# Kernel optimization log

Hardware: AMD Instinct MI355X
Metric: run time of the kernel (lower is better)

## Reference

```python
import jax, jax.numpy as jnp
import numpy as np

# Gemma3-style config (matches init_kwargs)
NUM_HEADS = 8
NUM_KV_GROUPS = 4
HEAD_DIM = 256
GROUP_SIZE = NUM_HEADS // NUM_KV_GROUPS
SLIDING_WINDOW = 1024
QUERY_PRE_ATTN_SCALAR = 256.0
SCALE = QUERY_PRE_ATTN_SCALAR ** (-0.5)
EPS = 1e-6


def rmsnorm(x, scale):
    # Gemma-style RMSNorm: fp32 variance, zero-centered weight with (1 + scale)
    xf = x.astype(jnp.float32)
    var = jnp.mean(xf * xf, axis=-1, keepdims=True)
    out = xf * jax.lax.rsqrt(var + EPS) * (1.0 + scale.astype(jnp.float32))
    return out.astype(x.dtype)


def sliding_causal_mask(q_len, kv_len, dtype):
    # additive mask [q_len, kv_len]: 0 allowed, -inf blocked
    q_pos = jnp.arange(kv_len - q_len, kv_len)[:, None]
    k_pos = jnp.arange(kv_len)[None, :]
    allowed = (k_pos <= q_pos) & (k_pos >= q_pos - SLIDING_WINDOW + 1)
    return jnp.where(allowed, jnp.zeros((), dtype), jnp.array(-jnp.inf, dtype))


def setup_inputs() -> dict:
    key = jax.random.key(0)
    ks = jax.random.split(key, 5)
    B, T, D = 2, 2048, 2560
    H, G, Hd = NUM_HEADS, NUM_KV_GROUPS, HEAD_DIM
    x = jax.random.normal(ks[0], (B, T, D), dtype=jnp.float32)
    Wq = jax.random.normal(ks[1], (D, H * Hd), dtype=jnp.float32) * 0.02
    Wk = jax.random.normal(ks[2], (D, G * Hd), dtype=jnp.float32) * 0.02
    Wv = jax.random.normal(ks[3], (D, G * Hd), dtype=jnp.float32) * 0.02
    Wo = jax.random.normal(ks[4], (H * Hd, D), dtype=jnp.float32) * 0.02
    q_scale = jnp.zeros((Hd,), dtype=jnp.float32)
    k_scale = jnp.zeros((Hd,), dtype=jnp.float32)
    return {"x": x, "Wq": Wq, "Wk": Wk, "Wv": Wv, "Wo": Wo,
            "q_scale": q_scale, "k_scale": k_scale}


def reference(x, Wq, Wk, Wv, Wo, q_scale, k_scale):
    B, T, D = x.shape
    H, G, g, Hd = NUM_HEADS, NUM_KV_GROUPS, GROUP_SIZE, HEAD_DIM
    # projections
    q = (x @ Wq).reshape(B, T, H, Hd).transpose(0, 2, 1, 3)   # [B,H,T,Hd]
    k = (x @ Wk).reshape(B, T, G, Hd).transpose(0, 2, 1, 3)   # [B,G,T,Hd]
    v = (x @ Wv).reshape(B, T, G, Hd).transpose(0, 2, 1, 3)   # [B,G,T,Hd]
    # qk-norm
    q = rmsnorm(q, q_scale)
    k = rmsnorm(k, k_scale)
    S = T  # no past_kv (prefill)
    # faithful reproduction of the module's head-group reshapes
    q = q.reshape(B, G, g, T, Hd).reshape(B * g, G, T, Hd)
    k = jnp.broadcast_to(k[:, None], (B, g, G, S, Hd)).reshape(B * g, G, S, Hd)
    v = jnp.broadcast_to(v[:, None], (B, g, G, S, Hd)).reshape(B * g, G, S, Hd)
    mask = sliding_causal_mask(T, S, q.dtype)  # [T,S]
    scores = jnp.einsum('bgtd,bgsd->bgts', q, k) * SCALE + mask
    attn = jax.nn.softmax(scores, axis=-1)
    out = jnp.einsum('bgts,bgsd->bgtd', attn, v)
    # faithful inverse reshapes (note g/G order swap vs input, as in source)
    out = out.reshape(B, g, G, T, Hd).reshape(B, H, T, Hd)
    out = out.transpose(0, 2, 1, 3).reshape(B, T, H * Hd)
    return out @ Wo
```

## Files before the change

### kernel.cpp

```cpp
#include <hip/hip_runtime.h>
#include <hip/hip_bf16.h>

typedef unsigned short u16;

#define T_SEQ 2048
#define NTOK 4096
#define D_MODEL 2560
#define NQKV 4096
#define WIN 1024
#define ATTN_SCALE 0.0625f
#define SMAX 17.0f
#define KROW 264
#define VROW 40

typedef __attribute__((ext_vector_type(8))) short bf16x8;
typedef __attribute__((ext_vector_type(8))) unsigned short u16x8;
typedef __attribute__((ext_vector_type(4))) float f32x4;

__device__ __forceinline__ float bf2f(u16 u) {
  union { unsigned int i; float f; } c; c.i = ((unsigned int)u) << 16; return c.f;
}
__device__ __forceinline__ u16 f2bf(float f) {
  __hip_bfloat16 h = __float2bfloat16(f);
  return __builtin_bit_cast(u16, h);
}
__device__ __forceinline__ u16x8 load8f(const float* p) {
  float4 a = *(const float4*)p;
  float4 b = *(const float4*)(p + 4);
  u16x8 r;
  r[0] = f2bf(a.x); r[1] = f2bf(a.y); r[2] = f2bf(a.z); r[3] = f2bf(a.w);
  r[4] = f2bf(b.x); r[5] = f2bf(b.y); r[6] = f2bf(b.z); r[7] = f2bf(b.w);
  return r;
}
__device__ __forceinline__ void gload_lds16(const u16* g, u16* l) {
  __builtin_amdgcn_global_load_lds(
      (const __attribute__((address_space(1))) void*)g,
      (__attribute__((address_space(3))) void*)l, 16, 0, 0);
}

__global__ __launch_bounds__(256) void cvt_f32_bf16(
    const float* __restrict__ in, u16* __restrict__ out) {
  size_t i = ((size_t)blockIdx.x * 256 + threadIdx.x) * 8;
  *(u16x8*)(out + i) = load8f(in + i);
}

__global__ __launch_bounds__(256) void transpose_w(
    const float* __restrict__ in, u16* __restrict__ out, int K, int N) {
  __shared__ u16 tile[64][65];
  int kb = blockIdx.y * 64, nb = blockIdx.x * 64;
  int t = threadIdx.x;
  int c4 = (t & 15) * 4;
  int r0 = t >> 4;
#pragma unroll
  for (int i = 0; i < 4; ++i) {
    int r = r0 + i * 16;
    float4 v = *(const float4*)(in + (size_t)(kb + r) * N + nb + c4);
    tile[r][c4] = f2bf(v.x); tile[r][c4 + 1] = f2bf(v.y);
    tile[r][c4 + 2] = f2bf(v.z); tile[r][c4 + 3] = f2bf(v.w);
  }
  __syncthreads();
#pragma unroll
  for (int i = 0; i < 4; ++i) {
    int n = r0 + i * 16;
    ushort4 v;
    v.x = tile[c4 + 0][n];
    v.y = tile[c4 + 1][n];
    v.z = tile[c4 + 2][n];
    v.w = tile[c4 + 3][n];
    *(ushort4*)(out + (size_t)(nb + n) * K + kb + c4) = v;
  }
}

__global__ __launch_bounds__(256) void v_transpose(
    const u16* __restrict__ qkv, u16* __restrict__ Vt) {
  int bg = blockIdx.z; int b = bg >> 2, g = bg & 3;
  __shared__ u16 tile[64][65];
  int tb = blockIdx.y * 64, db = blockIdx.x * 64;
  const u16* in = qkv + (size_t)(b * T_SEQ) * NQKV + 3072 + g * 256;
  u16* out = Vt + (size_t)bg * 256 * T_SEQ;
  int t = threadIdx.x;
  int c4 = (t & 15) * 4;
  int r0 = t >> 4;
#pragma unroll
  for (int i = 0; i < 4; ++i) {
    int r = r0 + i * 16;
    ushort4 v = *(const ushort4*)(in + (size_t)(tb + r) * NQKV + db + c4);
    tile[r][c4] = v.x; tile[r][c4 + 1] = v.y; tile[r][c4 + 2] = v.z; tile[r][c4 + 3] = v.w;
  }
  __syncthreads();
#pragma unroll
  for (int i = 0; i < 4; ++i) {
    int n = r0 + i * 16;
    ushort4 v;
    v.x = tile[c4 + 0][n];
    v.y = tile[c4 + 1][n];
    v.z = tile[c4 + 2][n];
    v.w = tile[c4 + 3][n];
    *(ushort4*)(out + (size_t)(db + n) * T_SEQ + tb + c4) = v;
  }
}

template <int WC>
__global__ __launch_bounds__(512, 2) void gemm_256(
    const u16* __restrict__ A, int lda, const u16* __restrict__ Bt, int ldb,
    void* __restrict__ C, int ldc, int K) {
  extern __shared__ ulong2 LDSraw[];
  u16* SA = (u16*)LDSraw;
  u16* SB = SA + 32768;
  const int tid = threadIdx.x;
  const int wave = tid >> 6, lane = tid & 63;
  const int quad = lane >> 4, l16 = lane & 15;
  const int gx = gridDim.x;
  const int orig = blockIdx.y * gx + blockIdx.x;
  const int cpx = (gx * gridDim.y) >> 3;
  const int swz = (orig & 7) * cpx + (orig >> 3);
  const int mblk = (swz / gx) * 256, nblk = (swz % gx) * 256;
  const int wm = (wave >> 2) * 128, wn = (wave & 3) * 64;

  const u16* srcA[2]; const u16* srcB[2];
  int ldsOff[2];
#pragma unroll
  for (int i = 0; i < 2; ++i) {
    int u = i * 512 + tid;
    int hi3 = (u & 7) ^ ((u >> 3) & 7);
    int r = ((u >> 3) << 1) | (hi3 >> 2);
    int cbe = (hi3 & 3) << 3;
    srcA[i] = A + (size_t)(mblk + r) * lda + cbe;
    srcB[i] = Bt + (size_t)(nblk + r) * ldb + cbe;
    ldsOff[i] = (u >> 6) << 9;
  }
  const int unit = ((((l16 & 1) << 2) | quad) ^ ((l16 >> 1) & 7)) << 3;
  const int base_a = ((wm >> 1) + (l16 >> 1)) * 64 + unit;
  const int base_b = ((wn >> 1) + (l16 >> 1)) * 64 + unit;
  const int NK = K >> 5;
  f32x4 acc[8][4] = {};

  auto stage = [&](int s, int i) {
    int slot = s & 3;
    gload_lds16(srcA[i] + s * 32, SA + slot * 8192 + ldsOff[i]);
    gload_lds16(srcB[i] + s * 32, SB + slot * 8192 + ldsOff[i]);
  };

  stage(0, 0); stage(0, 1); stage(1, 0); stage(1, 1); stage(2, 0); stage(2, 1);
  asm volatile("s_waitcnt vmcnt(8)" ::: "memory");
  __builtin_amdgcn_s_barrier();
  asm volatile("" ::: "memory");

  for (int s = 0; s < NK; ++s) {
    const u16* sa = SA + (s & 3) * 8192;
    const u16* sb = SB + (s & 3) * 8192;
    bf16x8 aF[4], bF[4];
#pragma unroll
    for (int t = 0; t < 4; ++t) aF[t] = *(const bf16x8*)(sa + base_a + t * 512);
#pragma unroll
    for (int t = 0; t < 4; ++t) bF[t] = *(const bf16x8*)(sb + base_b + t * 512);
    if (s + 3 < NK) stage(s + 3, 0);
    asm volatile("" ::: "memory");
    __builtin_amdgcn_s_barrier();
    asm volatile("s_waitcnt lgkmcnt(0)" ::: "memory");
    __builtin_amdgcn_sched_barrier(0);
    __builtin_amdgcn_s_setprio(1);
#pragma unroll
    for (int n = 0; n < 4; ++n)
#pragma unroll
      for (int m = 0; m < 4; ++m)
        acc[m][n] = __builtin_amdgcn_mfma_f32_16x16x32_bf16(aF[m], bF[n], acc[m][n], 0, 0, 0);
    __builtin_amdgcn_s_setprio(0);
    asm volatile("" ::: "memory");
    __builtin_amdgcn_s_barrier();
    asm volatile("" ::: "memory");
#pragma unroll
    for (int t = 0; t < 4; ++t) aF[t] = *(const bf16x8*)(sa + base_a + (t + 4) * 512);
    if (s + 3 < NK) stage(s + 3, 1);
    asm volatile("" ::: "memory");
    __builtin_amdgcn_s_barrier();
    asm volatile("s_waitcnt lgkmcnt(0)" ::: "memory");
    __builtin_amdgcn_sched_barrier(0);
    __builtin_amdgcn_s_setprio(1);
#pragma unroll
    for (int n = 0; n < 4; ++n)
#pragma unroll
      for (int m = 0; m < 4; ++m)
        acc[m + 4][n] = __builtin_amdgcn_mfma_f32_16x16x32_bf16(aF[m], bF[n], acc[m + 4][n], 0, 0, 0);
    __builtin_amdgcn_s_setprio(0);
    if (s < NK - 3)       asm volatile("s_waitcnt vmcnt(6)" ::: "memory");
    else if (s == NK - 3) asm volatile("s_waitcnt vmcnt(4)" ::: "memory");
    else if (s == NK - 2) asm volatile("s_waitcnt vmcnt(0)" ::: "memory");
    if (s + 1 < NK) {
      asm volatile("" ::: "memory");
      __builtin_amdgcn_s_barrier();
      asm volatile("" ::: "memory");
    }
  }
#pragma unroll
  for (int m = 0; m < 8; ++m)
#pragma unroll
    for (int n = 0; n < 4; ++n)
#pragma unroll
      for (int r = 0; r < 4; ++r) {
        int row = mblk + wm + m * 16 + quad * 4 + r;
        int col = nblk + wn + n * 16 + l16;
        if constexpr (WC)
          ((float*)C)[(size_t)row * ldc + col] = acc[m][n][r];
        else
          ((u16*)C)[(size_t)row * ldc + col] = f2bf(acc[m][n][r]);
      }
}

template <int WC>
__global__ __launch_bounds__(256, 2) void gemm_fast(
    const u16* __restrict__ A, int lda, const u16* __restrict__ Bt, int ldb,
    void* __restrict__ C, int ldc, int K) {
  __shared__ __align__(16) u16 As[128 * 32];
  __shared__ __align__(16) u16 Bs[128 * 32];
  const int tid = threadIdx.x;
  const int wave = tid >> 6, lane = tid & 63;
  const int quad = lane >> 4, l16 = lane & 15;
  const int mblk = blockIdx.y * 128, nblk = blockIdx.x * 128;
  const int wm = (wave >> 1) * 64, wn = (wave & 1) * 64;
  f32x4 acc[4][4] = {};
  const int c0 = wave * 2;
  for (int k0 = 0; k0 < K; k0 += 32) {
#pragma unroll
    for (int i = 0; i < 2; ++i) {
      int c = c0 + i;
      int flat = c * 64 + lane;
      int row = flat >> 2;
      int kb = (flat & 3) * 8;
      gload_lds16(A + (size_t)(mblk + row) * lda + k0 + kb, As + c * 512);
      gload_lds16(Bt + (size_t)(nblk + row) * ldb + k0 + kb, Bs + c * 512);
    }
    __syncthreads();
    bf16x8 aF[4], bF[4];
#pragma unroll
    for (int t = 0; t < 4; ++t) {
      aF[t] = *(const bf16x8*)(As + (wm + t * 16 + l16) * 32 + quad * 8);
      bF[t] = *(const bf16x8*)(Bs + (wn + t * 16 + l16) * 32 + quad * 8);
    }
#pragma unroll
    for (int tm = 0; tm < 4; ++tm)
#pragma unroll
      for (int tn = 0; tn < 4; ++tn)
        acc[tm][tn] = __builtin_amdgcn_mfma_f32_16x16x32_bf16(aF[tm], bF[tn], acc[tm][tn], 0, 0, 0);
    __syncthreads();
  }
#pragma unroll
  for (int tm = 0; tm < 4; ++tm)
#pragma unroll
    for (int tn = 0; tn < 4; ++tn)
#pragma unroll
      for (int r = 0; r < 4; ++r) {
        int row = mblk + wm + tm * 16 + quad * 4 + r;
        int col = nblk + wn + tn * 16 + l16;
        if constexpr (WC)
          ((float*)C)[(size_t)row * ldc + col] = acc[tm][tn][r];
        else
          ((u16*)C)[(size_t)row * ldc + col] = f2bf(acc[tm][tn][r]);
      }
}

__global__ __launch_bounds__(256, 2) void gemm_f32a(
    const float* __restrict__ A, int lda, const u16* __restrict__ Bt, int ldb,
    u16* __restrict__ C, int ldc, int K) {
  __shared__ __align__(16) u16 As[128 * 32];
  __shared__ __align__(16) u16 Bs[128 * 32];
  const int tid = threadIdx.x;
  const int wave = tid >> 6, lane = tid & 63;
  const int quad = lane >> 4, l16 = lane & 15;
  const int mblk = blockIdx.y * 128, nblk = blockIdx.x * 128;
  const int wm = (wave >> 1) * 64, wn = (wave & 1) * 64;
  f32x4 acc[4][4] = {};
  for (int k0 = 0; k0 < K; k0 += 32) {
#pragma unroll
    for (int i = 0; i < 2; ++i) {
      int u = i * 256 + tid;
      int row = u >> 2;
      int kb = (u & 3) * 8;
      *(u16x8*)(As + row * 32 + kb) = load8f(A + (size_t)(mblk + row) * lda + k0 + kb);
      *(u16x8*)(Bs + row * 32 + kb) = *(const u16x8*)(Bt + (size_t)(nblk + row) * ldb + k0 + kb);
    }
    __syncthreads();
    bf16x8 aF[4], bF[4];
#pragma unroll
    for (int t = 0; t < 4; ++t) {
      aF[t] = *(const bf16x8*)(As + (wm + t * 16 + l16) * 32 + quad * 8);
      bF[t] = *(const bf16x8*)(Bs + (wn + t * 16 + l16) * 32 + quad * 8);
    }
#pragma unroll
    for (int tm = 0; tm < 4; ++tm)
#pragma unroll
      for (int tn = 0; tn < 4; ++tn)
        acc[tm][tn] = __builtin_amdgcn_mfma_f32_16x16x32_bf16(aF[tm], bF[tn], acc[tm][tn], 0, 0, 0);
    __syncthreads();
  }
#pragma unroll
  for (int tm = 0; tm < 4; ++tm)
#pragma unroll
    for (int tn = 0; tn < 4; ++tn)
#pragma unroll
      for (int r = 0; r < 4; ++r) {
        int row = mblk + wm + tm * 16 + quad * 4 + r;
        int col = nblk + wn + tn * 16 + l16;
        C[(size_t)row * ldc + col] = f2bf(acc[tm][tn][r]);
      }
}

__global__ __launch_bounds__(256) void rmsnorm_qk(
    u16* __restrict__ qkv, const float* __restrict__ q_scale,
    const float* __restrict__ k_scale) {
  int wv = blockIdx.x * 4 + (threadIdx.x >> 6);
  int lane = threadIdx.x & 63;
  int token = wv / 12, j = wv - token * 12;
  const float* sc = (j < 8) ? q_scale : k_scale;
  int col = (j < 8) ? j * 256 : 2048 + (j - 8) * 256;
  u16* p = qkv + (size_t)token * NQKV + col;
  int d = lane * 4;
  ushort4 raw = *(const ushort4*)(p + d);
  float x0 = bf2f(raw.x), x1 = bf2f(raw.y), x2 = bf2f(raw.z), x3 = bf2f(raw.w);
  float sum = x0 * x0 + x1 * x1 + x2 * x2 + x3 * x3;
#pragma unroll
  for (int m = 1; m < 64; m <<= 1) sum += __shfl_xor(sum, m, 64);
  float r = rsqrtf(sum * (1.0f / 256.0f) + 1e-6f);
  float4 sv = *(const float4*)(sc + d);
  ushort4 o;
  o.x = f2bf(x0 * r * (1.0f + sv.x));
  o.y = f2bf(x1 * r * (1.0f + sv.y));
  o.z = f2bf(x2 * r * (1.0f + sv.z));
  o.w = f2bf(x3 * r * (1.0f + sv.w));
  *(ushort4*)(p + d) = o;
}

__global__ __launch_bounds__(256) void attn_fused(
    u16* __restrict__ qkv, const u16* __restrict__ Vt) {
  const int qt = blockIdx.x, h = blockIdx.y, b = blockIdx.z;
  const int g = h & 3;
  const int tid = threadIdx.x;
  const int wave = tid >> 6, lane = tid & 63;
  const int quad = lane >> 4, l16 = lane & 15;
  const int t0 = qt * 64;
  const int tw = t0 + wave * 16;
  __shared__ __align__(16) u16 Ks[2][32 * KROW];
  __shared__ __align__(16) u16 Vs[2][256 * VROW];
  __shared__ __align__(16) u16 Ps[4][16 * VROW];
  bf16x8 qF[8];
  {
    const u16* qrow = qkv + (size_t)(b * T_SEQ + tw + l16) * NQKV + h * 256;
#pragma unroll
    for (int kc = 0; kc < 8; ++kc)
      qF[kc] = *(const bf16x8*)(qrow + kc * 32 + quad * 8);
  }
  const u16* vt_base = Vt + (size_t)(b * 4 + g) * 256 * T_SEQ;
  const u16* k_base = qkv + (size_t)(b * T_SEQ) * NQKV + 2048 + g * 256;
  f32x4 o[16] = {};
  float lsum[4] = {0.f, 0.f, 0.f, 0.f};
  int s_lo = t0 - (WIN - 1); if (s_lo < 0) s_lo = 0; s_lo &= ~31;
  const int s_hi = t0 + 63;
  const int n_tiles = (s_hi - s_lo + 32) >> 5;

  u16x8 rK[4], rV[4];
#define ISSUE_LOADS(sb)                                                       \
  {                                                                           \
    _Pragma("unroll")                                                         \
    for (int i = 0; i < 4; ++i) {                                             \
      int u = i * 256 + tid;                                                  \
      int krow = u >> 5, kcb = u & 31;                                        \
      rK[i] = *(const u16x8*)(k_base + (size_t)((sb) + krow) * NQKV + kcb * 8);\
      int dim = u >> 2, kvp = (u & 3) * 8;                                    \
      rV[i] = *(const u16x8*)(vt_base + (size_t)dim * T_SEQ + (sb) + kvp);    \
    }                                                                         \
  }
#define WRITE_LDS(buf)                                                        \
  {                                                                           \
    _Pragma("unroll")                                                         \
    for (int i = 0; i < 4; ++i) {                                             \
      int u = i * 256 + tid;                                                  \
      int krow = u >> 5, kcb = u & 31;                                        \
      *(u16x8*)(Ks[buf] + krow * KROW + kcb * 8) = rK[i];                     \
      int dim = u >> 2, kvp = (u & 3) * 8;                                    \
      *(u16x8*)(Vs[buf] + dim * VROW + kvp) = rV[i];                          \
    }                                                                         \
  }

  ISSUE_LOADS(s_lo);
  WRITE_LDS(0);
  __syncthreads();

  for (int ti = 0; ti < n_tiles; ++ti) {
    const int sb = s_lo + ti * 32;
    const int buf = ti & 1;
    if (ti + 1 < n_tiles) ISSUE_LOADS(sb + 32);
    f32x4 st[2] = {};
#pragma unroll
    for (int nt = 0; nt < 2; ++nt)
#pragma unroll
      for (int kc = 0; kc < 8; ++kc) {
        bf16x8 kF = *(const bf16x8*)(Ks[buf] + (nt * 16 + l16) * KROW + kc * 32 + quad * 8);
        st[nt] = __builtin_amdgcn_mfma_f32_16x16x32_bf16(qF[kc], kF, st[nt], 0, 0, 0);
      }
    const bool full = (sb + 31 <= tw) && (sb >= tw + 15 - (WIN - 1));
#pragma unroll
    for (int r = 0; r < 4; ++r) {
      float v0 = st[0][r] * ATTN_SCALE - SMAX;
      float v1 = st[1][r] * ATTN_SCALE - SMAX;
      if (!full) {
        int t = tw + quad * 4 + r;
        int c0s = sb + l16, c1s = c0s + 16;
        v0 = (c0s <= t && c0s > t - WIN) ? v0 : -3.0e38f;
        v1 = (c1s <= t && c1s > t - WIN) ? v1 : -3.0e38f;
      }
      float p0 = __expf(v0);
      float p1 = __expf(v1);
      Ps[wave][(quad * 4 + r) * VROW + l16] = f2bf(p0);
      Ps[wave][(quad * 4 + r) * VROW + 16 + l16] = f2bf(p1);
      lsum[r] += p0 + p1;
    }
    bf16x8 pF = *(const bf16x8*)(&Ps[wave][l16 * VROW + quad * 8]);
#pragma unroll
    for (int nt = 0; nt < 16; ++nt) {
      bf16x8 vF = *(const bf16x8*)(Vs[buf] + (nt * 16 + l16) * VROW + quad * 8);
      o[nt] = __builtin_amdgcn_mfma_f32_16x16x32_bf16(pF, vF, o[nt], 0, 0, 0);
    }
    if (ti + 1 < n_tiles) WRITE_LDS(buf ^ 1);
    __syncthreads();
  }
#undef ISSUE_LOADS
#undef WRITE_LDS
#pragma unroll
  for (int r = 0; r < 4; ++r) {
    float s = lsum[r];
    s += __shfl_xor(s, 1, 64);
    s += __shfl_xor(s, 2, 64);
    s += __shfl_xor(s, 4, 64);
    s += __shfl_xor(s, 8, 64);
    lsum[r] = s;
  }
#pragma unroll
  for (int r = 0; r < 4; ++r) {
    float inv = 1.0f / lsum[r];
    int t = tw + quad * 4 + r;
    u16* orow = qkv + (size_t)(b * T_SEQ + t) * NQKV + h * 256;
#pragma unroll
    for (int nt = 0; nt < 16; ++nt)
      orow[nt * 16 + l16] = f2bf(o[nt][r] * inv);
  }
}

extern "C" void kernel_launch(void* const* d_in, const int* in_sizes, int n_in,
                              void* d_out, int out_size, void* d_ws, size_t ws_size,
                              hipStream_t stream) {
  const float* x       = (const float*)d_in[0];
  const float* Wq      = (const float*)d_in[1];
  const float* Wk      = (const float*)d_in[2];
  const float* Wv      = (const float*)d_in[3];
  const float* Wo      = (const float*)d_in[4];
  const float* q_scale = (const float*)d_in[5];
  const float* k_scale = (const float*)d_in[6];

  u16* qkv = (u16*)d_ws;
  const size_t BIG_WS = (size_t)NTOK * NQKV * 2
                      + (size_t)NTOK * D_MODEL * 2
                      + (size_t)NQKV * D_MODEL * 2;

  if (ws_size >= BIG_WS) {
    (void)hipFuncSetAttribute(reinterpret_cast<const void*>(&gemm_256<0>),
                              hipFuncAttributeMaxDynamicSharedMemorySize, 131072);
    u16* xbf = qkv + (size_t)NTOK * NQKV;
    u16* WT  = xbf + (size_t)NTOK * D_MODEL;
    cvt_f32_bf16<<<dim3(NTOK * D_MODEL / (256 * 8)), 256, 0, stream>>>(x, xbf);
    transpose_w<<<dim3(32, 40), 256, 0, stream>>>(Wq, WT, D_MODEL, 2048);
    transpose_w<<<dim3(16, 40), 256, 0, stream>>>(Wk, WT + (size_t)2048 * D_MODEL, D_MODEL, 1024);
    transpose_w<<<dim3(16, 40), 256, 0, stream>>>(Wv, WT + (size_t)3072 * D_MODEL, D_MODEL, 1024);
    gemm_256<0><<<dim3(16, 16), 512, 131072, stream>>>(xbf, D_MODEL, WT, D_MODEL, qkv, NQKV, D_MODEL);
    rmsnorm_qk<<<dim3(12288), 256, 0, stream>>>(qkv, q_scale, k_scale);
    v_transpose<<<dim3(4, 32, 8), 256, 0, stream>>>(qkv, xbf);
    attn_fused<<<dim3(T_SEQ / 64, 8, 2), 256, 0, stream>>>(qkv, xbf);
    transpose_w<<<dim3(40, 32), 256, 0, stream>>>(Wo, WT, 2048, D_MODEL);
    gemm_fast<1><<<dim3(20, 32), 256, 0, stream>>>(qkv, NQKV, WT, 2048, d_out, D_MODEL, 2048);
  } else {
    u16* WT = qkv + (size_t)NTOK * NQKV;
    transpose_w<<<dim3(32, 40), 256, 0, stream>>>(Wq, WT, D_MODEL, 2048);
    gemm_f32a<<<dim3(16, 32), 256, 0, stream>>>(x, D_MODEL, WT, D_MODEL, qkv, NQKV, D_MODEL);
    transpose_w<<<dim3(16, 40), 256, 0, stream>>>(Wk, WT, D_MODEL, 1024);
    gemm_f32a<<<dim3(8, 32), 256, 0, stream>>>(x, D_MODEL, WT, D_MODEL, qkv + 2048, NQKV, D_MODEL);
    transpose_w<<<dim3(16, 40), 256, 0, stream>>>(Wv, WT, D_MODEL, 1024);
    gemm_f32a<<<dim3(8, 32), 256, 0, stream>>>(x, D_MODEL, WT, D_MODEL, qkv + 3072, NQKV, D_MODEL);
    rmsnorm_qk<<<dim3(12288), 256, 0, stream>>>(qkv, q_scale, k_scale);
    v_transpose<<<dim3(4, 32, 8), 256, 0, stream>>>(qkv, WT);
    attn_fused<<<dim3(T_SEQ / 64, 8, 2), 256, 0, stream>>>(qkv, WT);
    transpose_w<<<dim3(40, 32), 256, 0, stream>>>(Wo, WT, 2048, D_MODEL);
    gemm_fast<1><<<dim3(20, 32), 256, 0, stream>>>(qkv, NQKV, WT, 2048, d_out, D_MODEL, 2048);
  }
}
```

Baseline: 378.6 us.

## Use 4-wave 256x256 GEMM with 128x128 per-wave tiles for QKV and output projections

Reworks the 256x256-tile GEMM from 8 waves with 128x64 per-wave tiles to 4 waves with 128x128 per-wave tiles. Each wave now holds 64 accumulator tiles and loads 8 A and 8 B fragments per k-step, which raises MFMA work per LDS read. The same kernel also replaces the 128-tile gemm_fast for the output projection, now on a 10x16 grid. The cost is much higher register pressure (launch_bounds 256,1) and fewer waves to hide latency, and the output GEMM launches only 160 blocks, which may underfill the device.

```diff
diff --git a/kernel.cpp b/kernel.cpp
--- a/kernel.cpp
+++ b/kernel.cpp
@@ -101,7 +101,7 @@
 }
 
 template <int WC>
-__global__ __launch_bounds__(512, 2) void gemm_256(
+__global__ __launch_bounds__(256, 1) void gemm_fat(
     const u16* __restrict__ A, int lda, const u16* __restrict__ Bt, int ldb,
     void* __restrict__ C, int ldc, int K) {
   extern __shared__ ulong2 LDSraw[];
@@ -115,13 +115,13 @@
   const int cpx = (gx * gridDim.y) >> 3;
   const int swz = (orig & 7) * cpx + (orig >> 3);
   const int mblk = (swz / gx) * 256, nblk = (swz % gx) * 256;
-  const int wm = (wave >> 2) * 128, wn = (wave & 3) * 64;
-
-  const u16* srcA[2]; const u16* srcB[2];
-  int ldsOff[2];
-#pragma unroll
-  for (int i = 0; i < 2; ++i) {
-    int u = i * 512 + tid;
+  const int wm = (wave >> 1) * 128, wn = (wave & 1) * 128;
+
+  const u16* srcA[4]; const u16* srcB[4];
+  int ldsOff[4];
+#pragma unroll
+  for (int i = 0; i < 4; ++i) {
+    int u = i * 256 + tid;
     int hi3 = (u & 7) ^ ((u >> 3) & 7);
     int r = ((u >> 3) << 1) | (hi3 >> 2);
     int cbe = (hi3 & 3) << 3;
@@ -133,28 +133,33 @@
   const int base_a = ((wm >> 1) + (l16 >> 1)) * 64 + unit;
   const int base_b = ((wn >> 1) + (l16 >> 1)) * 64 + unit;
   const int NK = K >> 5;
-  f32x4 acc[8][4] = {};
-
-  auto stage = [&](int s, int i) {
-    int slot = s & 3;
-    gload_lds16(srcA[i] + s * 32, SA + slot * 8192 + ldsOff[i]);
-    gload_lds16(srcB[i] + s * 32, SB + slot * 8192 + ldsOff[i]);
+  f32x4 acc[8][8] = {};
+
+  auto stageA = [&](int s) {
+    u16* d = SA + (s & 3) * 8192;
+#pragma unroll
+    for (int i = 0; i < 4; ++i) gload_lds16(srcA[i] + s * 32, d + ldsOff[i]);
   };
-
-  stage(0, 0); stage(0, 1); stage(1, 0); stage(1, 1); stage(2, 0); stage(2, 1);
-  asm volatile("s_waitcnt vmcnt(8)" ::: "memory");
+  auto stageB = [&](int s) {
+    u16* d = SB + (s & 3) * 8192;
+#pragma unroll
+    for (int i = 0; i < 4; ++i) gload_lds16(srcB[i] + s * 32, d + ldsOff[i]);
+  };
+
+  stageA(0); stageB(0); stageA(1); stageB(1); stageA(2); stageB(2);
+  asm volatile("s_waitcnt vmcnt(16)" ::: "memory");
   __builtin_amdgcn_s_barrier();
   asm volatile("" ::: "memory");
 
   for (int s = 0; s < NK; ++s) {
     const u16* sa = SA + (s & 3) * 8192;
     const u16* sb = SB + (s & 3) * 8192;
-    bf16x8 aF[4], bF[4];
-#pragma unroll
-    for (int t = 0; t < 4; ++t) aF[t] = *(const bf16x8*)(sa + base_a + t * 512);
+    bf16x8 aF[8], bF[8];
+#pragma unroll
+    for (int t = 0; t < 8; ++t) aF[t] = *(const bf16x8*)(sa + base_a + t * 512);
 #pragma unroll
     for (int t = 0; t < 4; ++t) bF[t] = *(const bf16x8*)(sb + base_b + t * 512);
-    if (s + 3 < NK) stage(s + 3, 0);
+    if (s + 3 < NK) stageA(s + 3);
     asm volatile("" ::: "memory");
     __builtin_amdgcn_s_barrier();
     asm volatile("s_waitcnt lgkmcnt(0)" ::: "memory");
@@ -163,28 +168,28 @@
 #pragma unroll
     for (int n = 0; n < 4; ++n)
 #pragma unroll
-      for (int m = 0; m < 4; ++m)
+      for (int m = 0; m < 8; ++m)
         acc[m][n] = __builtin_amdgcn_mfma_f32_16x16x32_bf16(aF[m], bF[n], acc[m][n], 0, 0, 0);
     __builtin_amdgcn_s_setprio(0);
     asm volatile("" ::: "memory");
     __builtin_amdgcn_s_barrier();
     asm volatile("" ::: "memory");
 #pragma unroll
-    for (int t = 0; t < 4; ++t) aF[t] = *(const bf16x8*)(sa + base_a + (t + 4) * 512);
-    if (s + 3 < NK) stage(s + 3, 1);
+    for (int t = 4; t < 8; ++t) bF[t] = *(const bf16x8*)(sb + base_b + t * 512);
+    if (s + 3 < NK) stageB(s + 3);
     asm volatile("" ::: "memory");
     __builtin_amdgcn_s_barrier();
     asm volatile("s_waitcnt lgkmcnt(0)" ::: "memory");
     __builtin_amdgcn_sched_barrier(0);
     __builtin_amdgcn_s_setprio(1);
 #pragma unroll
-    for (int n = 0; n < 4; ++n)
-#pragma unroll
-      for (int m = 0; m < 4; ++m)
-        acc[m + 4][n] = __builtin_amdgcn_mfma_f32_16x16x32_bf16(aF[m], bF[n], acc[m + 4][n], 0, 0, 0);
+    for (int n = 4; n < 8; ++n)
+#pragma unroll
+      for (int m = 0; m < 8; ++m)
+        acc[m][n] = __builtin_amdgcn_mfma_f32_16x16x32_bf16(aF[m], bF[n], acc[m][n], 0, 0, 0);
     __builtin_amdgcn_s_setprio(0);
-    if (s < NK - 3)       asm volatile("s_waitcnt vmcnt(6)" ::: "memory");
-    else if (s == NK - 3) asm volatile("s_waitcnt vmcnt(4)" ::: "memory");
+    if (s < NK - 3)       asm volatile("s_waitcnt vmcnt(16)" ::: "memory");
+    else if (s == NK - 3) asm volatile("s_waitcnt vmcnt(8)" ::: "memory");
     else if (s == NK - 2) asm volatile("s_waitcnt vmcnt(0)" ::: "memory");
     if (s + 1 < NK) {
       asm volatile("" ::: "memory");
@@ -195,7 +200,7 @@
 #pragma unroll
   for (int m = 0; m < 8; ++m)
 #pragma unroll
-    for (int n = 0; n < 4; ++n)
+    for (int n = 0; n < 8; ++n)
 #pragma unroll
       for (int r = 0; r < 4; ++r) {
         int row = mblk + wm + m * 16 + quad * 4 + r;
@@ -462,7 +467,9 @@
                       + (size_t)NQKV * D_MODEL * 2;
 
   if (ws_size >= BIG_WS) {
-    (void)hipFuncSetAttribute(reinterpret_cast<const void*>(&gemm_256<0>),
+    (void)hipFuncSetAttribute(reinterpret_cast<const void*>(&gemm_fat<0>),
+                              hipFuncAttributeMaxDynamicSharedMemorySize, 131072);
+    (void)hipFuncSetAttribute(reinterpret_cast<const void*>(&gemm_fat<1>),
                               hipFuncAttributeMaxDynamicSharedMemorySize, 131072);
     u16* xbf = qkv + (size_t)NTOK * NQKV;
     u16* WT  = xbf + (size_t)NTOK * D_MODEL;
@@ -470,12 +477,12 @@
     transpose_w<<<dim3(32, 40), 256, 0, stream>>>(Wq, WT, D_MODEL, 2048);
     transpose_w<<<dim3(16, 40), 256, 0, stream>>>(Wk, WT + (size_t)2048 * D_MODEL, D_MODEL, 1024);
     transpose_w<<<dim3(16, 40), 256, 0, stream>>>(Wv, WT + (size_t)3072 * D_MODEL, D_MODEL, 1024);
-    gemm_256<0><<<dim3(16, 16), 512, 131072, stream>>>(xbf, D_MODEL, WT, D_MODEL, qkv, NQKV, D_MODEL);
+    gemm_fat<0><<<dim3(16, 16), 256, 131072, stream>>>(xbf, D_MODEL, WT, D_MODEL, qkv, NQKV, D_MODEL);
     rmsnorm_qk<<<dim3(12288), 256, 0, stream>>>(qkv, q_scale, k_scale);
     v_transpose<<<dim3(4, 32, 8), 256, 0, stream>>>(qkv, xbf);
     attn_fused<<<dim3(T_SEQ / 64, 8, 2), 256, 0, stream>>>(qkv, xbf);
     transpose_w<<<dim3(40, 32), 256, 0, stream>>>(Wo, WT, 2048, D_MODEL);
-    gemm_fast<1><<<dim3(20, 32), 256, 0, stream>>>(qkv, NQKV, WT, 2048, d_out, D_MODEL, 2048);
+    gemm_fat<1><<<dim3(10, 16), 256, 131072, stream>>>(qkv, NQKV, WT, 2048, d_out, D_MODEL, 2048);
   } else {
     u16* WT = qkv + (size_t)NTOK * NQKV;
     transpose_w<<<dim3(32, 40), 256, 0, stream>>>(Wq, WT, D_MODEL, 2048);
```

Result: slower. 389.9 us (+3.0%).

## Restructure QKV GEMM main loop and merge small prep/post kernels

Applied to the files above, without the earlier changes.

The QKV GEMM inner loop now preloads the next step's first A fragments and loads the second half of A with B up front. This cuts the barriers and explicit lgkmcnt waits per K step from four to two, so LDS reads overlap with MFMA work. Separately, the input conversion and Wq/Wk/Wv transposes are merged into one `prep` launch. RMSNorm, the V transpose and the Wo transpose are merged into one `post` launch, removing several kernel launches and the gaps between them. The trade-off is more live fragment registers and looser LDS synchronisation in the GEMM, which could cost occupancy or introduce subtle ordering hazards.

```diff
diff --git a/kernel.cpp b/kernel.cpp
--- a/kernel.cpp
+++ b/kernel.cpp
@@ -38,17 +38,16 @@
       (__attribute__((address_space(3))) void*)l, 16, 0, 0);
 }
 
-__global__ __launch_bounds__(256) void cvt_f32_bf16(
-    const float* __restrict__ in, u16* __restrict__ out) {
-  size_t i = ((size_t)blockIdx.x * 256 + threadIdx.x) * 8;
+__device__ __forceinline__ void cvt_body(
+    const float* __restrict__ in, u16* __restrict__ out, int bid, int t) {
+  size_t i = ((size_t)bid * 256 + t) * 8;
   *(u16x8*)(out + i) = load8f(in + i);
 }
 
-__global__ __launch_bounds__(256) void transpose_w(
-    const float* __restrict__ in, u16* __restrict__ out, int K, int N) {
-  __shared__ u16 tile[64][65];
-  int kb = blockIdx.y * 64, nb = blockIdx.x * 64;
-  int t = threadIdx.x;
+__device__ __forceinline__ void tw_body(
+    const float* __restrict__ in, u16* __restrict__ out, int K, int N,
+    int bx, int by, int t, u16 (*tile)[65]) {
+  int kb = by * 64, nb = bx * 64;
   int c4 = (t & 15) * 4;
   int r0 = t >> 4;
 #pragma unroll
@@ -71,14 +70,13 @@
   }
 }
 
-__global__ __launch_bounds__(256) void v_transpose(
-    const u16* __restrict__ qkv, u16* __restrict__ Vt) {
-  int bg = blockIdx.z; int b = bg >> 2, g = bg & 3;
-  __shared__ u16 tile[64][65];
-  int tb = blockIdx.y * 64, db = blockIdx.x * 64;
+__device__ __forceinline__ void vt_body(
+    const u16* __restrict__ qkv, u16* __restrict__ Vt,
+    int bx, int by, int bg, int t, u16 (*tile)[65]) {
+  int b = bg >> 2, g = bg & 3;
+  int tb = by * 64, db = bx * 64;
   const u16* in = qkv + (size_t)(b * T_SEQ) * NQKV + 3072 + g * 256;
   u16* out = Vt + (size_t)bg * 256 * T_SEQ;
-  int t = threadIdx.x;
   int c4 = (t & 15) * 4;
   int r0 = t >> 4;
 #pragma unroll
@@ -98,6 +96,75 @@
     v.w = tile[c4 + 3][n];
     *(ushort4*)(out + (size_t)(db + n) * T_SEQ + tb + c4) = v;
   }
+}
+
+__device__ __forceinline__ void rms_body(
+    u16* __restrict__ qkv, const float* __restrict__ q_scale,
+    const float* __restrict__ k_scale, int bid, int tidx) {
+  int wv = bid * 4 + (tidx >> 6);
+  int lane = tidx & 63;
+  int token = wv / 12, j = wv - token * 12;
+  const float* sc = (j < 8) ? q_scale : k_scale;
+  int col = (j < 8) ? j * 256 : 2048 + (j - 8) * 256;
+  u16* p = qkv + (size_t)token * NQKV + col;
+  int d = lane * 4;
+  ushort4 raw = *(const ushort4*)(p + d);
+  float x0 = bf2f(raw.x), x1 = bf2f(raw.y), x2 = bf2f(raw.z), x3 = bf2f(raw.w);
+  float sum = x0 * x0 + x1 * x1 + x2 * x2 + x3 * x3;
+#pragma unroll
+  for (int m = 1; m < 64; m <<= 1) sum += __shfl_xor(sum, m, 64);
+  float r = rsqrtf(sum * (1.0f / 256.0f) + 1e-6f);
+  float4 sv = *(const float4*)(sc + d);
+  ushort4 o;
+  o.x = f2bf(x0 * r * (1.0f + sv.x));
+  o.y = f2bf(x1 * r * (1.0f + sv.y));
+  o.z = f2bf(x2 * r * (1.0f + sv.z));
+  o.w = f2bf(x3 * r * (1.0f + sv.w));
+  *(ushort4*)(p + d) = o;
+}
+
+__global__ __launch_bounds__(256) void prep(
+    const float* __restrict__ x, u16* __restrict__ xbf,
+    const float* __restrict__ Wq, const float* __restrict__ Wk,
+    const float* __restrict__ Wv, u16* __restrict__ WT) {
+  __shared__ u16 tile[64][65];
+  int id = blockIdx.x, t = threadIdx.x;
+  if (id < 5120) { cvt_body(x, xbf, id, t); return; }
+  id -= 5120;
+  if (id < 1280) { tw_body(Wq, WT, D_MODEL, 2048, id % 32, id / 32, t, tile); return; }
+  id -= 1280;
+  if (id < 640) { tw_body(Wk, WT + (size_t)2048 * D_MODEL, D_MODEL, 1024, id % 16, id / 16, t, tile); return; }
+  id -= 640;
+  tw_body(Wv, WT + (size_t)3072 * D_MODEL, D_MODEL, 1024, id % 16, id / 16, t, tile);
+}
+
+__global__ __launch_bounds__(256) void post(
+    u16* __restrict__ qkv, const float* __restrict__ q_scale,
+    const float* __restrict__ k_scale, u16* __restrict__ Vt,
+    const float* __restrict__ Wo, u16* __restrict__ WT) {
+  __shared__ u16 tile[64][65];
+  int id = blockIdx.x, t = threadIdx.x;
+  if (id < 12288) { rms_body(qkv, q_scale, k_scale, id, t); return; }
+  id -= 12288;
+  if (id < 1024) { vt_body(qkv, Vt, id & 3, (id >> 2) & 31, id >> 7, t, tile); return; }
+  id -= 1024;
+  tw_body(Wo, WT, 2048, D_MODEL, id % 40, id / 40, t, tile);
+}
+
+__global__ __launch_bounds__(256) void transpose_w(
+    const float* __restrict__ in, u16* __restrict__ out, int K, int N) {
+  __shared__ u16 tile[64][65];
+  tw_body(in, out, K, N, blockIdx.x, blockIdx.y, threadIdx.x, tile);
+}
+__global__ __launch_bounds__(256) void v_transpose(
+    const u16* __restrict__ qkv, u16* __restrict__ Vt) {
+  __shared__ u16 tile[64][65];
+  vt_body(qkv, Vt, blockIdx.x, blockIdx.y, blockIdx.z, threadIdx.x, tile);
+}
+__global__ __launch_bounds__(256) void rmsnorm_qk(
+    u16* __restrict__ qkv, const float* __restrict__ q_scale,
+    const float* __restrict__ k_scale) {
+  rms_body(qkv, q_scale, k_scale, blockIdx.x, threadIdx.x);
 }
 
 template <int WC>
@@ -146,46 +213,43 @@
   __builtin_amdgcn_s_barrier();
   asm volatile("" ::: "memory");
 
+  bf16x8 aA[4], aB[4], bF[4];
+#pragma unroll
+  for (int t = 0; t < 4; ++t) aA[t] = *(const bf16x8*)(SA + base_a + t * 512);
+
   for (int s = 0; s < NK; ++s) {
     const u16* sa = SA + (s & 3) * 8192;
     const u16* sb = SB + (s & 3) * 8192;
-    bf16x8 aF[4], bF[4];
-#pragma unroll
-    for (int t = 0; t < 4; ++t) aF[t] = *(const bf16x8*)(sa + base_a + t * 512);
 #pragma unroll
     for (int t = 0; t < 4; ++t) bF[t] = *(const bf16x8*)(sb + base_b + t * 512);
+#pragma unroll
+    for (int t = 0; t < 4; ++t) aB[t] = *(const bf16x8*)(sa + base_a + (t + 4) * 512);
     if (s + 3 < NK) stage(s + 3, 0);
-    asm volatile("" ::: "memory");
-    __builtin_amdgcn_s_barrier();
-    asm volatile("s_waitcnt lgkmcnt(0)" ::: "memory");
-    __builtin_amdgcn_sched_barrier(0);
     __builtin_amdgcn_s_setprio(1);
 #pragma unroll
     for (int n = 0; n < 4; ++n)
 #pragma unroll
       for (int m = 0; m < 4; ++m)
-        acc[m][n] = __builtin_amdgcn_mfma_f32_16x16x32_bf16(aF[m], bF[n], acc[m][n], 0, 0, 0);
-    __builtin_amdgcn_s_setprio(0);
-    asm volatile("" ::: "memory");
-    __builtin_amdgcn_s_barrier();
-    asm volatile("" ::: "memory");
-#pragma unroll
-    for (int t = 0; t < 4; ++t) aF[t] = *(const bf16x8*)(sa + base_a + (t + 4) * 512);
-    if (s + 3 < NK) stage(s + 3, 1);
-    asm volatile("" ::: "memory");
-    __builtin_amdgcn_s_barrier();
-    asm volatile("s_waitcnt lgkmcnt(0)" ::: "memory");
-    __builtin_amdgcn_sched_barrier(0);
-    __builtin_amdgcn_s_setprio(1);
-#pragma unroll
-    for (int n = 0; n < 4; ++n)
-#pragma unroll
-      for (int m = 0; m < 4; ++m)
-        acc[m + 4][n] = __builtin_amdgcn_mfma_f32_16x16x32_bf16(aF[m], bF[n], acc[m + 4][n], 0, 0, 0);
+        acc[m][n] = __builtin_amdgcn_mfma_f32_16x16x32_bf16(aA[m], bF[n], acc[m][n], 0, 0, 0);
     __builtin_amdgcn_s_setprio(0);
     if (s < NK - 3)       asm volatile("s_waitcnt vmcnt(6)" ::: "memory");
     else if (s == NK - 3) asm volatile("s_waitcnt vmcnt(4)" ::: "memory");
     else if (s == NK - 2) asm volatile("s_waitcnt vmcnt(0)" ::: "memory");
+    __builtin_amdgcn_s_barrier();
+    asm volatile("" ::: "memory");
+    if (s + 1 < NK) {
+      const u16* sn = SA + ((s + 1) & 3) * 8192;
+#pragma unroll
+      for (int t = 0; t < 4; ++t) aA[t] = *(const bf16x8*)(sn + base_a + t * 512);
+    }
+    if (s + 3 < NK) stage(s + 3, 1);
+    __builtin_amdgcn_s_setprio(1);
+#pragma unroll
+    for (int n = 0; n < 4; ++n)
+#pragma unroll
+      for (int m = 0; m < 4; ++m)
+        acc[m + 4][n] = __builtin_amdgcn_mfma_f32_16x16x32_bf16(aB[m], bF[n], acc[m + 4][n], 0, 0, 0);
+    __builtin_amdgcn_s_setprio(0);
     if (s + 1 < NK) {
       asm volatile("" ::: "memory");
       __builtin_amdgcn_s_barrier();
@@ -303,31 +367,6 @@
         int col = nblk + wn + tn * 16 + l16;
         C[(size_t)row * ldc + col] = f2bf(acc[tm][tn][r]);
       }
-}
-
-__global__ __launch_bounds__(256) void rmsnorm_qk(
-    u16* __restrict__ qkv, const float* __restrict__ q_scale,
-    const float* __restrict__ k_scale) {
-  int wv = blockIdx.x * 4 + (threadIdx.x >> 6);
-  int lane = threadIdx.x & 63;
-  int token = wv / 12, j = wv - token * 12;
-  const float* sc = (j < 8) ? q_scale : k_scale;
-  int col = (j < 8) ? j * 256 : 2048 + (j - 8) * 256;
-  u16* p = qkv + (size_t)token * NQKV + col;
-  int d = lane * 4;
-  ushort4 raw = *(const ushort4*)(p + d);
-  float x0 = bf2f(raw.x), x1 = bf2f(raw.y), x2 = bf2f(raw.z), x3 = bf2f(raw.w);
-  float sum = x0 * x0 + x1 * x1 + x2 * x2 + x3 * x3;
-#pragma unroll
-  for (int m = 1; m < 64; m <<= 1) sum += __shfl_xor(sum, m, 64);
-  float r = rsqrtf(sum * (1.0f / 256.0f) + 1e-6f);
-  float4 sv = *(const float4*)(sc + d);
-  ushort4 o;
-  o.x = f2bf(x0 * r * (1.0f + sv.x));
-  o.y = f2bf(x1 * r * (1.0f + sv.y));
-  o.z = f2bf(x2 * r * (1.0f + sv.z));
-  o.w = f2bf(x3 * r * (1.0f + sv.w));
-  *(ushort4*)(p + d) = o;
 }
 
 __global__ __launch_bounds__(256) void attn_fused(
@@ -466,15 +505,10 @@
                               hipFuncAttributeMaxDynamicSharedMemorySize, 131072);
     u16* xbf = qkv + (size_t)NTOK * NQKV;
     u16* WT  = xbf + (size_t)NTOK * D_MODEL;
-    cvt_f32_bf16<<<dim3(NTOK * D_MODEL / (256 * 8)), 256, 0, stream>>>(x, xbf);
-    transpose_w<<<dim3(32, 40), 256, 0, stream>>>(Wq, WT, D_MODEL, 2048);
-    transpose_w<<<dim3(16, 40), 256, 0, stream>>>(Wk, WT + (size_t)2048 * D_MODEL, D_MODEL, 1024);
-    transpose_w<<<dim3(16, 40), 256, 0, stream>>>(Wv, WT + (size_t)3072 * D_MODEL, D_MODEL, 1024);
+    prep<<<dim3(5120 + 1280 + 640 + 640), 256, 0, stream>>>(x, xbf, Wq, Wk, Wv, WT);
     gemm_256<0><<<dim3(16, 16), 512, 131072, stream>>>(xbf, D_MODEL, WT, D_MODEL, qkv, NQKV, D_MODEL);
-    rmsnorm_qk<<<dim3(12288), 256, 0, stream>>>(qkv, q_scale, k_scale);
-    v_transpose<<<dim3(4, 32, 8), 256, 0, stream>>>(qkv, xbf);
+    post<<<dim3(12288 + 1024 + 1280), 256, 0, stream>>>(qkv, q_scale, k_scale, xbf, Wo, WT);
     attn_fused<<<dim3(T_SEQ / 64, 8, 2), 256, 0, stream>>>(qkv, xbf);
-    transpose_w<<<dim3(40, 32), 256, 0, stream>>>(Wo, WT, 2048, D_MODEL);
     gemm_fast<1><<<dim3(20, 32), 256, 0, stream>>>(qkv, NQKV, WT, 2048, d_out, D_MODEL, 2048);
   } else {
     u16* WT = qkv + (size_t)NTOK * NQKV;
```

Measured after the change: 360.8 us. 1.05x faster.
